# Kernel optimization log

Measured on AMD Instinct MI355X. Metric: run time of the kernel, lower is better.

Reference implementation:

```python
import jax, jax.numpy as jnp
import numpy as np

IMG = 256      # image size implied by 8x8 grid * scale 32
THRE = 0.5
DIS = 4        # img_dislocate_size
B = 64


def _shift_map(s, size, dis):
    # Pixel-level coordinate map for the dislocated half: cell r starts at
    # max(r*s - dis, 0) (the torch while-loop clamps negative coords to 0).
    p = jnp.arange(size)
    base = jnp.maximum((p // s) * s - dis, 0)
    return base + p % s


def _cell_norm(x, g, s):
    # Per-cell (crop) min/max normalization, matching the per-crop
    # (t - min) / (max - min + 1e-5) in HeatMaptoImg.
    b = x.shape[0]
    v = x.reshape(b, 1, g, s, g, s)
    mn = v.min(axis=(3, 5), keepdims=True)
    mx = v.max(axis=(3, 5), keepdims=True)
    return ((v - mn) / (mx - mn + 1e-5)).reshape(b, 1, g * s, g * s)


def setup_inputs() -> dict:
    key = jax.random.key(0)
    ks = jax.random.split(key, 7)
    B2 = 2 * B
    return {
        "img": jax.random.uniform(ks[0], (B, 1, IMG, IMG), jnp.float32),
        "heat8": jax.random.uniform(ks[1], (B2, 1, 8, 8), jnp.float32),
        "heat16": jax.random.uniform(ks[2], (B2, 1, 16, 16), jnp.float32),
        "heat32": jax.random.uniform(ks[3], (B2, 1, 32, 32), jnp.float32),
        "seg8": jax.random.uniform(ks[4], (B2, 1, IMG, IMG), jnp.float32),
        "seg16": jax.random.uniform(ks[5], (B2, 1, IMG, IMG), jnp.float32),
        "seg32": jax.random.uniform(ks[6], (B2, 1, IMG, IMG), jnp.float32),
    }


def reference(img, heat8, heat16, heat32, seg8, seg16, seg32):
    Bv = img.shape[0]
    label = jnp.zeros((Bv, 1, IMG, IMG), img.dtype)
    cnt = jnp.zeros_like(label)
    crops = {}
    # fine grid (scale 8) processed first, matching the reversed loop order
    for heat, seg, g in ((heat32, seg32, 32), (heat16, seg16, 16), (heat8, seg8, 8)):
        s = IMG // g                      # crop / cell size for this scale
        mask = (heat > THRE).astype(img.dtype)          # (2B,1,g,g)
        mask_pix = jnp.repeat(jnp.repeat(mask, s, axis=2), s, axis=3)  # (2B,1,256,256)
        Y = _shift_map(s, IMG, DIS)
        # dislocated half crops come from the shifted image region
        img_d = img[:, :, Y[:, None], Y[None, :]]       # (B,1,256,256)
        both = jnp.concatenate([img, img_d], axis=0)    # (2B,1,256,256)
        crops[g] = _cell_norm(both, g, s) * mask_pix
        # UnitLabels: scatter-add per-crop labels + counts, then average
        ca = mask_pix[:Bv]
        label = label + ca * seg[:Bv]
        cnt = cnt + ca
        cd = mask_pix[Bv:]
        label = label.at[:, :, Y[:, None], Y[None, :]].add(cd * seg[Bv:])
        cnt = cnt.at[:, :, Y[:, None], Y[None, :]].add(cd)
    label = label / (cnt + 1e-10)
    return (crops[32], crops[16], crops[8], label)
```

## Files before the change

### kernel.cpp

```cpp
#include <hip/hip_runtime.h>

#define IMG   256
#define IMG2  65536
#define NB    64
#define NB2   128

#define NBLK_C8   2048
#define NBLK_C16  1024
#define NBLK_C32  512
#define NBLK_LBL  4096
#define NBLK_ALL  (NBLK_C8 + NBLK_C16 + NBLK_C32 + NBLK_LBL)

template <int S>
__device__ __forceinline__ void crops_cell_row(
    const float* __restrict__ img,
    const float* __restrict__ heat,
    float* __restrict__ out,
    int src, int ci,
    float (*s_red)[32][4],
    float (*s_fin)[4]) {
    constexpr int G   = IMG / S;
    constexpr int L   = (S == 8) ? 3 : (S == 16) ? 4 : 5;
    constexpr int CPL = S / 4;

    const int tid = threadIdx.x;
    const int w   = tid >> 6;
    const int l   = tid & 63;
    const int cj  = l >> (L - 2);
    const int o   = (l & (CPL - 1)) * 4;

    const int rA   = ci * S;
    const int rB   = (ci == 0) ? 0 : rA - 4;
    const int colA = cj * S + o;
    const int colB = ((cj == 0) ? 0 : cj * S - 4) + o;

    const float* __restrict__ sp = img + (size_t)src * IMG2;

    float mnA = 3.4e38f, mxA = -3.4e38f, mnB = 3.4e38f, mxB = -3.4e38f;
#pragma unroll
    for (int k = 0; k < S / 4; ++k) {
        const int r = w + 4 * k;
        const float4 a  = *(const float4*)(sp + (rA + r) * IMG + colA);
        const float4 bq = *(const float4*)(sp + (rB + r) * IMG + colB);
        mnA = fminf(mnA, fminf(fminf(a.x, a.y), fminf(a.z, a.w)));
        mxA = fmaxf(mxA, fmaxf(fmaxf(a.x, a.y), fmaxf(a.z, a.w)));
        mnB = fminf(mnB, fminf(fminf(bq.x, bq.y), fminf(bq.z, bq.w)));
        mxB = fmaxf(mxB, fmaxf(fmaxf(bq.x, bq.y), fmaxf(bq.z, bq.w)));
    }
#pragma unroll
    for (int off = 1; off < CPL; off <<= 1) {
        mnA = fminf(mnA, __shfl_xor(mnA, off, 64));
        mxA = fmaxf(mxA, __shfl_xor(mxA, off, 64));
        mnB = fminf(mnB, __shfl_xor(mnB, off, 64));
        mxB = fmaxf(mxB, __shfl_xor(mxB, off, 64));
    }
    if ((l & (CPL - 1)) == 0) {
        float* p = &s_red[w][cj][0];
        p[0] = mnA; p[1] = mxA; p[2] = mnB; p[3] = mxB;
    }
    __syncthreads();
    if (tid < G) {
        float a0 = 3.4e38f, a1 = -3.4e38f, b0 = 3.4e38f, b1 = -3.4e38f;
#pragma unroll
        for (int ww = 0; ww < 4; ++ww) {
            a0 = fminf(a0, s_red[ww][tid][0]);
            a1 = fmaxf(a1, s_red[ww][tid][1]);
            b0 = fminf(b0, s_red[ww][tid][2]);
            b1 = fmaxf(b1, s_red[ww][tid][3]);
        }
        const float hA = heat[(size_t)src * G * G + ci * G + tid];
        const float hB = heat[(size_t)(src + NB) * G * G + ci * G + tid];
        s_fin[tid][0] = a0;
        s_fin[tid][1] = (hA > 0.5f ? 1.0f : 0.0f) / (a1 - a0 + 1e-5f);
        s_fin[tid][2] = b0;
        s_fin[tid][3] = (hB > 0.5f ? 1.0f : 0.0f) / (b1 - b0 + 1e-5f);
    }
    __syncthreads();
    const float fmnA = s_fin[cj][0], finvA = s_fin[cj][1];
    const float fmnB = s_fin[cj][2], finvB = s_fin[cj][3];

    float* __restrict__ dA = out + (size_t)src * IMG2;
    float* __restrict__ dB = out + (size_t)(src + NB) * IMG2;
#pragma unroll
    for (int k = 0; k < S / 4; ++k) {
        const int r = w + 4 * k;
        const float4 a  = *(const float4*)(sp + (rA + r) * IMG + colA);
        const float4 bq = *(const float4*)(sp + (rB + r) * IMG + colB);
        float4 oa, ob;
        oa.x = (a.x - fmnA) * finvA;  oa.y = (a.y - fmnA) * finvA;
        oa.z = (a.z - fmnA) * finvA;  oa.w = (a.w - fmnA) * finvA;
        ob.x = (bq.x - fmnB) * finvB; ob.y = (bq.y - fmnB) * finvB;
        ob.z = (bq.z - fmnB) * finvB; ob.w = (bq.w - fmnB) * finvB;
        *(float4*)(dA + (rA + r) * IMG + colA) = oa;
        *(float4*)(dB + (rA + r) * IMG + colA) = ob;
    }
}

__device__ __forceinline__ void label_rows(
    const float* __restrict__ heat8,
    const float* __restrict__ heat16,
    const float* __restrict__ heat32,
    const float* __restrict__ seg8,
    const float* __restrict__ seg16,
    const float* __restrict__ seg32,
    float* __restrict__ out,
    int b, int u0) {
    const int wave = threadIdx.x >> 6;
    const int lane = threadIdx.x & 63;
    const int u    = u0 + wave;
    const int v0   = lane << 2;
    const int vs   = min(v0 + 4, 252);

    float nu[4] = {0.f, 0.f, 0.f, 0.f};
    float de[4] = {0.f, 0.f, 0.f, 0.f};

    if (u0 >= 32 && u0 <= 248) {
        const int i1 = u + 4;
#define SCALE_F(heat, seg, g, l, s)                                           \
        {                                                                     \
            const float* __restrict__ h1 = heat + b * (g * g);                \
            const float* __restrict__ h2 = heat + (NB + b) * (g * g);         \
            const float* __restrict__ r1 = seg + (size_t)b * IMG2 + u * IMG;  \
            const float* __restrict__ r2 =                                    \
                seg + (size_t)(NB + b) * IMG2 + i1 * IMG;                     \
            const float4 sd  = *(const float4*)(r1 + v0);                     \
            const float4 sg0 = *(const float4*)(r2 + v0);                     \
            const float4 sg1 = *(const float4*)(r2 + vs);                     \
            const float hd  = h1[(u >> l) * g + (v0 >> l)];                   \
            const float hg0 = h2[(i1 >> l) * g + (v0 >> l)];                  \
            const float hg1 = h2[(i1 >> l) * g + (vs >> l)];                  \
            const float md = (hd > 0.5f) ? 1.0f : 0.0f;                       \
            const float g0 = (hg0 > 0.5f) ? 1.0f : 0.0f;                      \
            const float g1 = (hg1 > 0.5f) ? 1.0f : 0.0f;                      \
            _Pragma("unroll")                                                 \
            for (int c = 0; c < 4; ++c) {                                     \
                const int v = v0 + c;                                         \
                const float m0 = (v < (s)) ? g0 : 0.0f;                       \
                const float m1 = (v >= (s) - 4 && v <= 251) ? g1 : 0.0f;      \
                float x = ((const float*)&sd)[c] * md;                        \
                x = fmaf(m0, ((const float*)&sg0)[c], x);                     \
                x = fmaf(m1, ((const float*)&sg1)[c], x);                     \
                nu[c] += x;                                                   \
                de[c] += md + m0 + m1;                                        \
            }                                                                 \
        }
        SCALE_F(heat32, seg32, 32, 3, 8)
        SCALE_F(heat16, seg16, 16, 4, 16)
        SCALE_F(heat8,  seg8,  8,  5, 32)
#undef SCALE_F
    } else {
        const int i0  = u;
        const int i1c = min(u + 4, 255);
#define SCALE_G(heat, seg, g, l, s)                                           \
        {                                                                     \
            const float* __restrict__ h1 = heat + b * (g * g);                \
            const float* __restrict__ h2 = heat + (NB + b) * (g * g);         \
            const float* __restrict__ r1 = seg + (size_t)b * IMG2 + u * IMG;  \
            const float* __restrict__ ra =                                    \
                seg + (size_t)(NB + b) * IMG2 + i0 * IMG;                     \
            const float* __restrict__ rb =                                    \
                seg + (size_t)(NB + b) * IMG2 + i1c * IMG;                    \
            const float4 sd  = *(const float4*)(r1 + v0);                     \
            const float4 a0q = *(const float4*)(ra + v0);                     \
            const float4 a1q = *(const float4*)(ra + vs);                     \
            const float4 b0q = *(const float4*)(rb + v0);                     \
            const float4 b1q = *(const float4*)(rb + vs);                     \
            const float hd  = h1[(u >> l) * g + (v0 >> l)];                   \
            const float hA0 = h2[(i0 >> l) * g + (v0 >> l)];                  \
            const float hA1 = h2[(i0 >> l) * g + (vs >> l)];                  \
            const float hB0 = h2[(i1c >> l) * g + (v0 >> l)];                 \
            const float hB1 = h2[(i1c >> l) * g + (vs >> l)];                 \
            const float miA = (u < (s)) ? 1.0f : 0.0f;                        \
            const float miB = (u >= (s) - 4 && u <= 251) ? 1.0f : 0.0f;       \
            const float md  = (hd > 0.5f) ? 1.0f : 0.0f;                      \
            const float gA0 = miA * ((hA0 > 0.5f) ? 1.0f : 0.0f);             \
            const float gA1 = miA * ((hA1 > 0.5f) ? 1.0f : 0.0f);             \
            const float gB0 = miB * ((hB0 > 0.5f) ? 1.0f : 0.0f);             \
            const float gB1 = miB * ((hB1 > 0.5f) ? 1.0f : 0.0f);             \
            _Pragma("unroll")                                                 \
            for (int c = 0; c < 4; ++c) {                                     \
                const int v = v0 + c;                                         \
                const float mj0 = (v < (s)) ? 1.0f : 0.0f;                    \
                const float mj1 = (v >= (s) - 4 && v <= 251) ? 1.0f : 0.0f;   \
                const float w00 = gA0 * mj0, w01 = gA1 * mj1;                 \
                const float w10 = gB0 * mj0, w11 = gB1 * mj1;                 \
                float x = ((const float*)&sd)[c] * md;                        \
                x = fmaf(w00, ((const float*)&a0q)[c], x);                    \
                x = fmaf(w01, ((const float*)&a1q)[c], x);                    \
                x = fmaf(w10, ((const float*)&b0q)[c], x);                    \
                x = fmaf(w11, ((const float*)&b1q)[c], x);                    \
                nu[c] += x;                                                   \
                de[c] += md + w00 + w01 + w10 + w11;                          \
            }                                                                 \
        }
        SCALE_G(heat32, seg32, 32, 3, 8)
        SCALE_G(heat16, seg16, 16, 4, 16)
        SCALE_G(heat8,  seg8,  8,  5, 32)
#undef SCALE_G
    }

    float4 o;
    o.x = nu[0] / (de[0] + 1e-10f);
    o.y = nu[1] / (de[1] + 1e-10f);
    o.z = nu[2] / (de[2] + 1e-10f);
    o.w = nu[3] / (de[3] + 1e-10f);
    *(float4*)(out + (size_t)b * IMG2 + u * IMG + v0) = o;
}

__global__ __launch_bounds__(256) void fused_kernel(
    const float* __restrict__ img,
    const float* __restrict__ heat8,
    const float* __restrict__ heat16,
    const float* __restrict__ heat32,
    const float* __restrict__ seg8,
    const float* __restrict__ seg16,
    const float* __restrict__ seg32,
    float* __restrict__ out) {
    __shared__ float s_red[4][32][4];
    __shared__ float s_fin[32][4];

    float* crops32 = out;
    float* crops16 = out + (size_t)NB2 * IMG2;
    float* crops8  = out + (size_t)2 * NB2 * IMG2;
    float* label   = out + (size_t)3 * NB2 * IMG2;

    const int bid = blockIdx.x;
    if (bid < NBLK_C8) {
        crops_cell_row<8>(img, heat32, crops32, bid >> 5, bid & 31, s_red, s_fin);
    } else if (bid < NBLK_C8 + NBLK_C16) {
        const int t = bid - NBLK_C8;
        crops_cell_row<16>(img, heat16, crops16, t >> 4, t & 15, s_red, s_fin);
    } else if (bid < NBLK_C8 + NBLK_C16 + NBLK_C32) {
        const int t = bid - (NBLK_C8 + NBLK_C16);
        crops_cell_row<32>(img, heat8, crops8, t >> 3, t & 7, s_red, s_fin);
    } else {
        const int t = bid - (NBLK_C8 + NBLK_C16 + NBLK_C32);
        label_rows(heat8, heat16, heat32, seg8, seg16, seg32, label,
                   t >> 6, (t & 63) << 2);
    }
}

extern "C" void kernel_launch(void* const* d_in, const int* in_sizes, int n_in,
                              void* d_out, int out_size, void* d_ws, size_t ws_size,
                              hipStream_t stream) {
    const float* img    = (const float*)d_in[0];
    const float* heat8  = (const float*)d_in[1];
    const float* heat16 = (const float*)d_in[2];
    const float* heat32 = (const float*)d_in[3];
    const float* seg8   = (const float*)d_in[4];
    const float* seg16  = (const float*)d_in[5];
    const float* seg32  = (const float*)d_in[6];

    fused_kernel<<<dim3(NBLK_ALL), 256, 0, stream>>>(
        img, heat8, heat16, heat32, seg8, seg16, seg32, (float*)d_out);
}
```

Measured before the change: 224.5 us.

## Interleave crop and label blocks, use nontemporal stores, raise occupancy hint

Remaps block indices so each group of 15 blocks mixes 7 crop-normalization blocks with 8 label blocks. This balances the read-heavy label work and the store-heavy crop work across the machine at the same time instead of running them as separate phases. All output writes become nontemporal vector stores so the streamed outputs do not pollute cache. The launch bounds add a minimum of 8 blocks per CU, which may force register limits or spills.

New measurement: 234.1 us. +4.3%, slower.

```diff
diff --git a/kernel.cpp b/kernel.cpp
--- a/kernel.cpp
+++ b/kernel.cpp
@@ -4,6 +4,13 @@
 #define IMG2  65536
 #define NB    64
 #define NB2   128
+
+typedef float v4f __attribute__((ext_vector_type(4)));
+
+__device__ __forceinline__ void nt_store4(float* p, float x, float y, float z, float w) {
+    v4f v = {x, y, z, w};
+    __builtin_nontemporal_store(v, (v4f*)p);
+}
 
 #define NBLK_C8   2048
 #define NBLK_C16  1024
@@ -86,13 +93,12 @@
         const int r = w + 4 * k;
         const float4 a  = *(const float4*)(sp + (rA + r) * IMG + colA);
         const float4 bq = *(const float4*)(sp + (rB + r) * IMG + colB);
-        float4 oa, ob;
-        oa.x = (a.x - fmnA) * finvA;  oa.y = (a.y - fmnA) * finvA;
-        oa.z = (a.z - fmnA) * finvA;  oa.w = (a.w - fmnA) * finvA;
-        ob.x = (bq.x - fmnB) * finvB; ob.y = (bq.y - fmnB) * finvB;
-        ob.z = (bq.z - fmnB) * finvB; ob.w = (bq.w - fmnB) * finvB;
-        *(float4*)(dA + (rA + r) * IMG + colA) = oa;
-        *(float4*)(dB + (rA + r) * IMG + colA) = ob;
+        nt_store4(dA + (rA + r) * IMG + colA,
+                  (a.x - fmnA) * finvA, (a.y - fmnA) * finvA,
+                  (a.z - fmnA) * finvA, (a.w - fmnA) * finvA);
+        nt_store4(dB + (rA + r) * IMG + colA,
+                  (bq.x - fmnB) * finvB, (bq.y - fmnB) * finvB,
+                  (bq.z - fmnB) * finvB, (bq.w - fmnB) * finvB);
     }
 }
 
@@ -199,15 +205,12 @@
 #undef SCALE_G
     }
 
-    float4 o;
-    o.x = nu[0] / (de[0] + 1e-10f);
-    o.y = nu[1] / (de[1] + 1e-10f);
-    o.z = nu[2] / (de[2] + 1e-10f);
-    o.w = nu[3] / (de[3] + 1e-10f);
-    *(float4*)(out + (size_t)b * IMG2 + u * IMG + v0) = o;
-}
-
-__global__ __launch_bounds__(256) void fused_kernel(
+    nt_store4(out + (size_t)b * IMG2 + u * IMG + v0,
+              nu[0] / (de[0] + 1e-10f), nu[1] / (de[1] + 1e-10f),
+              nu[2] / (de[2] + 1e-10f), nu[3] / (de[3] + 1e-10f));
+}
+
+__global__ __launch_bounds__(256, 8) void fused_kernel(
     const float* __restrict__ img,
     const float* __restrict__ heat8,
     const float* __restrict__ heat16,
@@ -225,18 +228,24 @@
     float* label   = out + (size_t)3 * NB2 * IMG2;
 
     const int bid = blockIdx.x;
-    if (bid < NBLK_C8) {
-        crops_cell_row<8>(img, heat32, crops32, bid >> 5, bid & 31, s_red, s_fin);
-    } else if (bid < NBLK_C8 + NBLK_C16) {
-        const int t = bid - NBLK_C8;
-        crops_cell_row<16>(img, heat16, crops16, t >> 4, t & 15, s_red, s_fin);
-    } else if (bid < NBLK_C8 + NBLK_C16 + NBLK_C32) {
-        const int t = bid - (NBLK_C8 + NBLK_C16);
-        crops_cell_row<32>(img, heat8, crops8, t >> 3, t & 7, s_red, s_fin);
+    const int grp = bid / 15;
+    const int rem = bid - grp * 15;
+
+    if (rem < 7) {
+        const int cid = grp * 7 + rem;
+        if (cid < NBLK_C8) {
+            crops_cell_row<8>(img, heat32, crops32, cid >> 5, cid & 31, s_red, s_fin);
+        } else if (cid < NBLK_C8 + NBLK_C16) {
+            const int t = cid - NBLK_C8;
+            crops_cell_row<16>(img, heat16, crops16, t >> 4, t & 15, s_red, s_fin);
+        } else {
+            const int t = cid - (NBLK_C8 + NBLK_C16);
+            crops_cell_row<32>(img, heat8, crops8, t >> 3, t & 7, s_red, s_fin);
+        }
     } else {
-        const int t = bid - (NBLK_C8 + NBLK_C16 + NBLK_C32);
+        const int lid = grp * 8 + (rem - 7);
         label_rows(heat8, heat16, heat32, seg8, seg16, seg32, label,
-                   t >> 6, (t & 63) << 2);
+                   lid >> 6, (lid & 63) << 2);
     }
 }
 
```

## Map each crop cell to one wavefront and interleave crop and label blocks

Applied to the files above, without the earlier changes.

Rewrites the crop normalization so that each 64-lane wavefront owns a whole cell, or a group of cells for scale 8. Min/max is reduced with wave shuffles only, which removes shared memory and the block-level __syncthreads. Loaded values stay in registers for the normalize pass instead of being read from global memory twice. The block schedule is also interleaved, 9 crop blocks then 4 label blocks in every group of 13, to mix memory-heavy work across the GPU. This raises register pressure in the scale-32 path, and the block-index arithmetic has to cover exactly 13312 blocks.

Result: no change. 224.2 us (-0.1%).

```diff
diff --git a/kernel.cpp b/kernel.cpp
--- a/kernel.cpp
+++ b/kernel.cpp
@@ -5,94 +5,146 @@
 #define NB    64
 #define NB2   128
 
-#define NBLK_C8   2048
-#define NBLK_C16  1024
-#define NBLK_C32  512
-#define NBLK_LBL  4096
-#define NBLK_ALL  (NBLK_C8 + NBLK_C16 + NBLK_C32 + NBLK_LBL)
-
-template <int S>
-__device__ __forceinline__ void crops_cell_row(
-    const float* __restrict__ img,
-    const float* __restrict__ heat,
-    float* __restrict__ out,
-    int src, int ci,
-    float (*s_red)[32][4],
-    float (*s_fin)[4]) {
-    constexpr int G   = IMG / S;
-    constexpr int L   = (S == 8) ? 3 : (S == 16) ? 4 : 5;
-    constexpr int CPL = S / 4;
-
-    const int tid = threadIdx.x;
-    const int w   = tid >> 6;
-    const int l   = tid & 63;
-    const int cj  = l >> (L - 2);
-    const int o   = (l & (CPL - 1)) * 4;
-
-    const int rA   = ci * S;
-    const int rB   = (ci == 0) ? 0 : rA - 4;
-    const int colA = cj * S + o;
-    const int colB = ((cj == 0) ? 0 : cj * S - 4) + o;
+#define NBLK_ALL  13312
+
+__device__ __forceinline__ float4 norm4(float4 a, float mn, float inv) {
+    float4 o;
+    o.x = (a.x - mn) * inv; o.y = (a.y - mn) * inv;
+    o.z = (a.z - mn) * inv; o.w = (a.w - mn) * inv;
+    return o;
+}
+
+__device__ __forceinline__ void mm4(float4 a, float& mn, float& mx) {
+    mn = fminf(mn, fminf(fminf(a.x, a.y), fminf(a.z, a.w)));
+    mx = fmaxf(mx, fmaxf(fmaxf(a.x, a.y), fmaxf(a.z, a.w)));
+}
+
+__device__ __forceinline__ void crops_s8(
+    const float* __restrict__ img, const float* __restrict__ heat,
+    float* __restrict__ out, int wid) {
+    const int l   = threadIdx.x & 63;
+    const int src = wid >> 8;
+    const int rem = wid & 255;
+    const int ci  = rem >> 3;
+    const int st  = rem & 7;
+
+    const int r    = l >> 3;
+    const int cj   = st * 4 + ((l >> 1) & 3);
+    const int o    = (l & 1) * 4;
+    const int rowA = ci * 8 + r;
+    const int rowB = ((ci == 0) ? 0 : ci * 8 - 4) + r;
+    const int colA = st * 32 + (l & 7) * 4;
+    const int colB = ((cj == 0) ? 0 : cj * 8 - 4) + o;
 
     const float* __restrict__ sp = img + (size_t)src * IMG2;
+    const float4 a  = *(const float4*)(sp + rowA * IMG + colA);
+    const float4 bq = *(const float4*)(sp + rowB * IMG + colB);
 
     float mnA = 3.4e38f, mxA = -3.4e38f, mnB = 3.4e38f, mxB = -3.4e38f;
-#pragma unroll
-    for (int k = 0; k < S / 4; ++k) {
-        const int r = w + 4 * k;
-        const float4 a  = *(const float4*)(sp + (rA + r) * IMG + colA);
-        const float4 bq = *(const float4*)(sp + (rB + r) * IMG + colB);
-        mnA = fminf(mnA, fminf(fminf(a.x, a.y), fminf(a.z, a.w)));
-        mxA = fmaxf(mxA, fmaxf(fmaxf(a.x, a.y), fmaxf(a.z, a.w)));
-        mnB = fminf(mnB, fminf(fminf(bq.x, bq.y), fminf(bq.z, bq.w)));
-        mxB = fmaxf(mxB, fmaxf(fmaxf(bq.x, bq.y), fmaxf(bq.z, bq.w)));
-    }
-#pragma unroll
-    for (int off = 1; off < CPL; off <<= 1) {
+    mm4(a, mnA, mxA); mm4(bq, mnB, mxB);
+#pragma unroll
+    for (int k = 0; k < 4; ++k) {
+        const int off = (k == 0) ? 1 : (4 << k);
         mnA = fminf(mnA, __shfl_xor(mnA, off, 64));
         mxA = fmaxf(mxA, __shfl_xor(mxA, off, 64));
         mnB = fminf(mnB, __shfl_xor(mnB, off, 64));
         mxB = fmaxf(mxB, __shfl_xor(mxB, off, 64));
     }
-    if ((l & (CPL - 1)) == 0) {
-        float* p = &s_red[w][cj][0];
-        p[0] = mnA; p[1] = mxA; p[2] = mnB; p[3] = mxB;
-    }
-    __syncthreads();
-    if (tid < G) {
-        float a0 = 3.4e38f, a1 = -3.4e38f, b0 = 3.4e38f, b1 = -3.4e38f;
-#pragma unroll
-        for (int ww = 0; ww < 4; ++ww) {
-            a0 = fminf(a0, s_red[ww][tid][0]);
-            a1 = fmaxf(a1, s_red[ww][tid][1]);
-            b0 = fminf(b0, s_red[ww][tid][2]);
-            b1 = fmaxf(b1, s_red[ww][tid][3]);
-        }
-        const float hA = heat[(size_t)src * G * G + ci * G + tid];
-        const float hB = heat[(size_t)(src + NB) * G * G + ci * G + tid];
-        s_fin[tid][0] = a0;
-        s_fin[tid][1] = (hA > 0.5f ? 1.0f : 0.0f) / (a1 - a0 + 1e-5f);
-        s_fin[tid][2] = b0;
-        s_fin[tid][3] = (hB > 0.5f ? 1.0f : 0.0f) / (b1 - b0 + 1e-5f);
-    }
-    __syncthreads();
-    const float fmnA = s_fin[cj][0], finvA = s_fin[cj][1];
-    const float fmnB = s_fin[cj][2], finvB = s_fin[cj][3];
+    const float hA = heat[(size_t)src * 1024 + ci * 32 + cj];
+    const float hB = heat[(size_t)(src + NB) * 1024 + ci * 32 + cj];
+    const float invA = (hA > 0.5f ? 1.0f : 0.0f) / (mxA - mnA + 1e-5f);
+    const float invB = (hB > 0.5f ? 1.0f : 0.0f) / (mxB - mnB + 1e-5f);
+
+    const size_t p = (size_t)src * IMG2 + rowA * IMG + colA;
+    *(float4*)(out + p)                      = norm4(a,  mnA, invA);
+    *(float4*)(out + p + (size_t)NB * IMG2)  = norm4(bq, mnB, invB);
+}
+
+__device__ __forceinline__ void crops_s16(
+    const float* __restrict__ img, const float* __restrict__ heat,
+    float* __restrict__ out, int wid) {
+    const int l   = threadIdx.x & 63;
+    const int src = wid >> 8;
+    const int rem = wid & 255;
+    const int ci  = rem >> 4;
+    const int cj  = rem & 15;
+
+    const int r    = l >> 2;
+    const int o    = (l & 3) * 4;
+    const int rowA = ci * 16 + r;
+    const int rowB = ((ci == 0) ? 0 : ci * 16 - 4) + r;
+    const int colA = cj * 16 + o;
+    const int colB = ((cj == 0) ? 0 : cj * 16 - 4) + o;
+
+    const float* __restrict__ sp = img + (size_t)src * IMG2;
+    const float4 a  = *(const float4*)(sp + rowA * IMG + colA);
+    const float4 bq = *(const float4*)(sp + rowB * IMG + colB);
+
+    float mnA = 3.4e38f, mxA = -3.4e38f, mnB = 3.4e38f, mxB = -3.4e38f;
+    mm4(a, mnA, mxA); mm4(bq, mnB, mxB);
+#pragma unroll
+    for (int off = 1; off < 64; off <<= 1) {
+        mnA = fminf(mnA, __shfl_xor(mnA, off, 64));
+        mxA = fmaxf(mxA, __shfl_xor(mxA, off, 64));
+        mnB = fminf(mnB, __shfl_xor(mnB, off, 64));
+        mxB = fmaxf(mxB, __shfl_xor(mxB, off, 64));
+    }
+    const float hA = heat[(size_t)src * 256 + ci * 16 + cj];
+    const float hB = heat[(size_t)(src + NB) * 256 + ci * 16 + cj];
+    const float invA = (hA > 0.5f ? 1.0f : 0.0f) / (mxA - mnA + 1e-5f);
+    const float invB = (hB > 0.5f ? 1.0f : 0.0f) / (mxB - mnB + 1e-5f);
+
+    const size_t p = (size_t)src * IMG2 + rowA * IMG + colA;
+    *(float4*)(out + p)                      = norm4(a,  mnA, invA);
+    *(float4*)(out + p + (size_t)NB * IMG2)  = norm4(bq, mnB, invB);
+}
+
+__device__ __forceinline__ void crops_s32(
+    const float* __restrict__ img, const float* __restrict__ heat,
+    float* __restrict__ out, int wid) {
+    const int l   = threadIdx.x & 63;
+    const int src = wid >> 6;
+    const int rem = wid & 63;
+    const int ci  = rem >> 3;
+    const int cj  = rem & 7;
+
+    const int r0   = l >> 3;
+    const int o    = (l & 7) * 4;
+    const int rA   = ci * 32;
+    const int rB   = (ci == 0) ? 0 : rA - 4;
+    const int colA = cj * 32 + o;
+    const int colB = ((cj == 0) ? 0 : cj * 32 - 4) + o;
+
+    const float* __restrict__ sp = img + (size_t)src * IMG2;
+    float4 a[4], bq[4];
+#pragma unroll
+    for (int k = 0; k < 4; ++k) {
+        const int r = r0 + 8 * k;
+        a[k]  = *(const float4*)(sp + (rA + r) * IMG + colA);
+        bq[k] = *(const float4*)(sp + (rB + r) * IMG + colB);
+    }
+    float mnA = 3.4e38f, mxA = -3.4e38f, mnB = 3.4e38f, mxB = -3.4e38f;
+#pragma unroll
+    for (int k = 0; k < 4; ++k) { mm4(a[k], mnA, mxA); mm4(bq[k], mnB, mxB); }
+#pragma unroll
+    for (int off = 1; off < 64; off <<= 1) {
+        mnA = fminf(mnA, __shfl_xor(mnA, off, 64));
+        mxA = fmaxf(mxA, __shfl_xor(mxA, off, 64));
+        mnB = fminf(mnB, __shfl_xor(mnB, off, 64));
+        mxB = fmaxf(mxB, __shfl_xor(mxB, off, 64));
+    }
+    const float hA = heat[(size_t)src * 64 + ci * 8 + cj];
+    const float hB = heat[(size_t)(src + NB) * 64 + ci * 8 + cj];
+    const float invA = (hA > 0.5f ? 1.0f : 0.0f) / (mxA - mnA + 1e-5f);
+    const float invB = (hB > 0.5f ? 1.0f : 0.0f) / (mxB - mnB + 1e-5f);
 
     float* __restrict__ dA = out + (size_t)src * IMG2;
     float* __restrict__ dB = out + (size_t)(src + NB) * IMG2;
 #pragma unroll
-    for (int k = 0; k < S / 4; ++k) {
-        const int r = w + 4 * k;
-        const float4 a  = *(const float4*)(sp + (rA + r) * IMG + colA);
-        const float4 bq = *(const float4*)(sp + (rB + r) * IMG + colB);
-        float4 oa, ob;
-        oa.x = (a.x - fmnA) * finvA;  oa.y = (a.y - fmnA) * finvA;
-        oa.z = (a.z - fmnA) * finvA;  oa.w = (a.w - fmnA) * finvA;
-        ob.x = (bq.x - fmnB) * finvB; ob.y = (bq.y - fmnB) * finvB;
-        ob.z = (bq.z - fmnB) * finvB; ob.w = (bq.w - fmnB) * finvB;
-        *(float4*)(dA + (rA + r) * IMG + colA) = oa;
-        *(float4*)(dB + (rA + r) * IMG + colA) = ob;
+    for (int k = 0; k < 4; ++k) {
+        const int r = r0 + 8 * k;
+        *(float4*)(dA + (rA + r) * IMG + colA) = norm4(a[k],  mnA, invA);
+        *(float4*)(dB + (rA + r) * IMG + colA) = norm4(bq[k], mnB, invB);
     }
 }
 
@@ -216,27 +268,29 @@
     const float* __restrict__ seg16,
     const float* __restrict__ seg32,
     float* __restrict__ out) {
-    __shared__ float s_red[4][32][4];
-    __shared__ float s_fin[32][4];
-
     float* crops32 = out;
     float* crops16 = out + (size_t)NB2 * IMG2;
     float* crops8  = out + (size_t)2 * NB2 * IMG2;
     float* label   = out + (size_t)3 * NB2 * IMG2;
 
     const int bid = blockIdx.x;
-    if (bid < NBLK_C8) {
-        crops_cell_row<8>(img, heat32, crops32, bid >> 5, bid & 31, s_red, s_fin);
-    } else if (bid < NBLK_C8 + NBLK_C16) {
-        const int t = bid - NBLK_C8;
-        crops_cell_row<16>(img, heat16, crops16, t >> 4, t & 15, s_red, s_fin);
-    } else if (bid < NBLK_C8 + NBLK_C16 + NBLK_C32) {
-        const int t = bid - (NBLK_C8 + NBLK_C16);
-        crops_cell_row<32>(img, heat8, crops8, t >> 3, t & 7, s_red, s_fin);
+    const int grp = bid / 13;
+    const int rem = bid - grp * 13;
+
+    if (rem < 9) {
+        const int cb  = grp * 9 + rem;
+        const int wid = cb * 4 + (threadIdx.x >> 6);
+        if (cb < 4096) {
+            crops_s8(img, heat32, crops32, wid);
+        } else if (cb < 8192) {
+            crops_s16(img, heat16, crops16, wid - 16384);
+        } else {
+            crops_s32(img, heat8, crops8, wid - 32768);
+        }
     } else {
-        const int t = bid - (NBLK_C8 + NBLK_C16 + NBLK_C32);
+        const int lid = grp * 4 + (rem - 9);
         label_rows(heat8, heat16, heat32, seg8, seg16, seg32, label,
-                   t >> 6, (t & 63) << 2);
+                   lid >> 6, (lid & 63) << 2);
     }
 }
 
```

## Split crops into stats pass plus row-streaming normalize kernel, separate label kernel

Applied to the files above, without the earlier changes.

Replaces the per-cell-row crops blocks with two stages. A stats kernel computes per-cell min and scaled inverse range into workspace, one thread per cell. A row-streaming kernel then reads each image row once and writes the normalized outputs for all three scales. The label work moves into its own launch. This trades one fused launch for three launches plus a workspace round trip, aiming for fully coalesced row-wise writes and fewer redundant image reads. The stats kernel's one-thread-per-cell serial loops (up to 32x32 values per thread) could be slow and poorly coalesced.

Result: slower. 250.3 us (+11.5%).

```diff
diff --git a/kernel.cpp b/kernel.cpp
--- a/kernel.cpp
+++ b/kernel.cpp
@@ -5,95 +5,119 @@
 #define NB    64
 #define NB2   128
 
-#define NBLK_C8   2048
-#define NBLK_C16  1024
-#define NBLK_C32  512
-#define NBLK_LBL  4096
-#define NBLK_ALL  (NBLK_C8 + NBLK_C16 + NBLK_C32 + NBLK_LBL)
-
-template <int S>
-__device__ __forceinline__ void crops_cell_row(
+
+#define WS_A8   0
+#define WS_B8   65536
+#define WS_A16  131072
+#define WS_B16  147456
+#define WS_A32  163840
+#define WS_B32  167936
+
+template <int S, int G>
+__device__ __forceinline__ void cell_stats(
+    const float* __restrict__ img, const float* __restrict__ heat,
+    float2* __restrict__ ws, int idx, int half, int wsbase) {
+    const int b  = idx / (G * G);
+    const int rr = idx % (G * G);
+    const int ci = rr / G;
+    const int cj = rr % G;
+    const int r0 = half ? max(ci * S - 4, 0) : ci * S;
+    const int c0 = half ? max(cj * S - 4, 0) : cj * S;
+    const float* __restrict__ p = img + (size_t)b * IMG2 + r0 * IMG + c0;
+    float mn = 3.4e38f, mx = -3.4e38f;
+    for (int r = 0; r < S; ++r) {
+#pragma unroll
+        for (int c = 0; c < S; c += 4) {
+            const float4 q = *(const float4*)(p + r * IMG + c);
+            mn = fminf(mn, fminf(fminf(q.x, q.y), fminf(q.z, q.w)));
+            mx = fmaxf(mx, fmaxf(fmaxf(q.x, q.y), fmaxf(q.z, q.w)));
+        }
+    }
+    const float h   = heat[(size_t)(b + half * NB) * (G * G) + ci * G + cj];
+    const float inv = (h > 0.5f ? 1.0f : 0.0f) / (mx - mn + 1e-5f);
+    ws[wsbase + idx] = make_float2(mn, inv);
+}
+
+__global__ __launch_bounds__(256) void stats_kernel(
     const float* __restrict__ img,
-    const float* __restrict__ heat,
-    float* __restrict__ out,
-    int src, int ci,
-    float (*s_red)[32][4],
-    float (*s_fin)[4]) {
-    constexpr int G   = IMG / S;
-    constexpr int L   = (S == 8) ? 3 : (S == 16) ? 4 : 5;
-    constexpr int CPL = S / 4;
-
-    const int tid = threadIdx.x;
-    const int w   = tid >> 6;
-    const int l   = tid & 63;
-    const int cj  = l >> (L - 2);
-    const int o   = (l & (CPL - 1)) * 4;
-
-    const int rA   = ci * S;
-    const int rB   = (ci == 0) ? 0 : rA - 4;
-    const int colA = cj * S + o;
-    const int colB = ((cj == 0) ? 0 : cj * S - 4) + o;
-
-    const float* __restrict__ sp = img + (size_t)src * IMG2;
-
-    float mnA = 3.4e38f, mxA = -3.4e38f, mnB = 3.4e38f, mxB = -3.4e38f;
-#pragma unroll
-    for (int k = 0; k < S / 4; ++k) {
-        const int r = w + 4 * k;
-        const float4 a  = *(const float4*)(sp + (rA + r) * IMG + colA);
-        const float4 bq = *(const float4*)(sp + (rB + r) * IMG + colB);
-        mnA = fminf(mnA, fminf(fminf(a.x, a.y), fminf(a.z, a.w)));
-        mxA = fmaxf(mxA, fmaxf(fmaxf(a.x, a.y), fmaxf(a.z, a.w)));
-        mnB = fminf(mnB, fminf(fminf(bq.x, bq.y), fminf(bq.z, bq.w)));
-        mxB = fmaxf(mxB, fmaxf(fmaxf(bq.x, bq.y), fmaxf(bq.z, bq.w)));
+    const float* __restrict__ heat8,
+    const float* __restrict__ heat16,
+    const float* __restrict__ heat32,
+    float2* __restrict__ ws) {
+    const int t = blockIdx.x * 256 + threadIdx.x;
+    if (t < 131072) {
+        const int half = t >> 16;
+        cell_stats<8, 32>(img, heat32, ws, t & 65535, half,
+                          half ? WS_B8 : WS_A8);
+    } else if (t < 163840) {
+        const int tt = t - 131072;
+        const int half = tt >> 14;
+        cell_stats<16, 16>(img, heat16, ws, tt & 16383, half,
+                           half ? WS_B16 : WS_A16);
+    } else {
+        const int tt = t - 163840;
+        const int half = tt >> 12;
+        cell_stats<32, 8>(img, heat8, ws, tt & 4095, half,
+                          half ? WS_B32 : WS_A32);
     }
-#pragma unroll
-    for (int off = 1; off < CPL; off <<= 1) {
-        mnA = fminf(mnA, __shfl_xor(mnA, off, 64));
-        mxA = fmaxf(mxA, __shfl_xor(mxA, off, 64));
-        mnB = fminf(mnB, __shfl_xor(mnB, off, 64));
-        mxB = fmaxf(mxB, __shfl_xor(mxB, off, 64));
-    }
-    if ((l & (CPL - 1)) == 0) {
-        float* p = &s_red[w][cj][0];
-        p[0] = mnA; p[1] = mxA; p[2] = mnB; p[3] = mxB;
-    }
-    __syncthreads();
-    if (tid < G) {
-        float a0 = 3.4e38f, a1 = -3.4e38f, b0 = 3.4e38f, b1 = -3.4e38f;
-#pragma unroll
-        for (int ww = 0; ww < 4; ++ww) {
-            a0 = fminf(a0, s_red[ww][tid][0]);
-            a1 = fmaxf(a1, s_red[ww][tid][1]);
-            b0 = fminf(b0, s_red[ww][tid][2]);
-            b1 = fmaxf(b1, s_red[ww][tid][3]);
-        }
-        const float hA = heat[(size_t)src * G * G + ci * G + tid];
-        const float hB = heat[(size_t)(src + NB) * G * G + ci * G + tid];
-        s_fin[tid][0] = a0;
-        s_fin[tid][1] = (hA > 0.5f ? 1.0f : 0.0f) / (a1 - a0 + 1e-5f);
-        s_fin[tid][2] = b0;
-        s_fin[tid][3] = (hB > 0.5f ? 1.0f : 0.0f) / (b1 - b0 + 1e-5f);
-    }
-    __syncthreads();
-    const float fmnA = s_fin[cj][0], finvA = s_fin[cj][1];
-    const float fmnB = s_fin[cj][2], finvB = s_fin[cj][3];
-
-    float* __restrict__ dA = out + (size_t)src * IMG2;
-    float* __restrict__ dB = out + (size_t)(src + NB) * IMG2;
-#pragma unroll
-    for (int k = 0; k < S / 4; ++k) {
-        const int r = w + 4 * k;
-        const float4 a  = *(const float4*)(sp + (rA + r) * IMG + colA);
-        const float4 bq = *(const float4*)(sp + (rB + r) * IMG + colB);
-        float4 oa, ob;
-        oa.x = (a.x - fmnA) * finvA;  oa.y = (a.y - fmnA) * finvA;
-        oa.z = (a.z - fmnA) * finvA;  oa.w = (a.w - fmnA) * finvA;
-        ob.x = (bq.x - fmnB) * finvB; ob.y = (bq.y - fmnB) * finvB;
-        ob.z = (bq.z - fmnB) * finvB; ob.w = (bq.w - fmnB) * finvB;
-        *(float4*)(dA + (rA + r) * IMG + colA) = oa;
-        *(float4*)(dB + (rA + r) * IMG + colA) = ob;
-    }
+}
+
+__device__ __forceinline__ float4 nrm(float4 q, float2 st) {
+    float4 o;
+    o.x = (q.x - st.x) * st.y; o.y = (q.y - st.x) * st.y;
+    o.z = (q.z - st.x) * st.y; o.w = (q.w - st.x) * st.y;
+    return o;
+}
+
+__global__ __launch_bounds__(256) void crops_stream_kernel(
+    const float* __restrict__ img,
+    const float2* __restrict__ ws,
+    float* __restrict__ out) {
+    const int w    = threadIdx.x >> 6;
+    const int lane = threadIdx.x & 63;
+    const int lid  = blockIdx.x * 4 + w;
+    const int b    = lid >> 8;
+    const int u    = lid & 255;
+    const int v0   = lane << 2;
+    const int vm   = max(v0 - 4, 0);
+
+    const float* __restrict__ ip = img + (size_t)b * IMG2;
+
+    const int u8  = ((u >> 3) ? (u & ~7)  - 4 : 0) + (u & 7);
+    const int u16 = ((u >> 4) ? (u & ~15) - 4 : 0) + (u & 15);
+    const int u32 = ((u >> 5) ? (u & ~31) - 4 : 0) + (u & 31);
+
+    const float4 xa  = *(const float4*)(ip + u   * IMG + v0);
+    const float4 q08 = *(const float4*)(ip + u8  * IMG + v0);
+    const float4 qm8 = *(const float4*)(ip + u8  * IMG + vm);
+    const float4 q16 = *(const float4*)(ip + u16 * IMG + v0);
+    const float4 qm6 = *(const float4*)(ip + u16 * IMG + vm);
+    const float4 q32 = *(const float4*)(ip + u32 * IMG + v0);
+    const float4 qm2 = *(const float4*)(ip + u32 * IMG + vm);
+
+    const float2 a8  = ws[WS_A8  + ((b << 5) + (u >> 3)) * 32 + (v0 >> 3)];
+    const float2 b8  = ws[WS_B8  + ((b << 5) + (u >> 3)) * 32 + (v0 >> 3)];
+    const float2 a16 = ws[WS_A16 + ((b << 4) + (u >> 4)) * 16 + (v0 >> 4)];
+    const float2 b16 = ws[WS_B16 + ((b << 4) + (u >> 4)) * 16 + (v0 >> 4)];
+    const float2 a32 = ws[WS_A32 + ((b << 3) + (u >> 5)) *  8 + (v0 >> 5)];
+    const float2 b32 = ws[WS_B32 + ((b << 3) + (u >> 5)) *  8 + (v0 >> 5)];
+
+    const float4 s8v = (v0 < 8)  ? q08 : qm8;
+    const float4 s16v = (v0 < 16) ? q16 : qm6;
+    const float4 s32v = (v0 < 32) ? q32 : qm2;
+
+    const size_t rowA = (size_t)b * IMG2 + u * IMG + v0;
+    const size_t rowB = (size_t)(b + NB) * IMG2 + u * IMG + v0;
+    float* __restrict__ c32 = out;
+    float* __restrict__ c16 = out + (size_t)NB2 * IMG2;
+    float* __restrict__ c8  = out + (size_t)2 * NB2 * IMG2;
+
+    *(float4*)(c32 + rowA) = nrm(xa,  a8);
+    *(float4*)(c32 + rowB) = nrm(s8v, b8);
+    *(float4*)(c16 + rowA) = nrm(xa,  a16);
+    *(float4*)(c16 + rowB) = nrm(s16v, b16);
+    *(float4*)(c8  + rowA) = nrm(xa,  a32);
+    *(float4*)(c8  + rowB) = nrm(s32v, b32);
 }
 
 __device__ __forceinline__ void label_rows(
@@ -207,8 +231,7 @@
     *(float4*)(out + (size_t)b * IMG2 + u * IMG + v0) = o;
 }
 
-__global__ __launch_bounds__(256) void fused_kernel(
-    const float* __restrict__ img,
+__global__ __launch_bounds__(256) void label_kernel(
     const float* __restrict__ heat8,
     const float* __restrict__ heat16,
     const float* __restrict__ heat32,
@@ -216,28 +239,10 @@
     const float* __restrict__ seg16,
     const float* __restrict__ seg32,
     float* __restrict__ out) {
-    __shared__ float s_red[4][32][4];
-    __shared__ float s_fin[32][4];
-
-    float* crops32 = out;
-    float* crops16 = out + (size_t)NB2 * IMG2;
-    float* crops8  = out + (size_t)2 * NB2 * IMG2;
-    float* label   = out + (size_t)3 * NB2 * IMG2;
-
-    const int bid = blockIdx.x;
-    if (bid < NBLK_C8) {
-        crops_cell_row<8>(img, heat32, crops32, bid >> 5, bid & 31, s_red, s_fin);
-    } else if (bid < NBLK_C8 + NBLK_C16) {
-        const int t = bid - NBLK_C8;
-        crops_cell_row<16>(img, heat16, crops16, t >> 4, t & 15, s_red, s_fin);
-    } else if (bid < NBLK_C8 + NBLK_C16 + NBLK_C32) {
-        const int t = bid - (NBLK_C8 + NBLK_C16);
-        crops_cell_row<32>(img, heat8, crops8, t >> 3, t & 7, s_red, s_fin);
-    } else {
-        const int t = bid - (NBLK_C8 + NBLK_C16 + NBLK_C32);
-        label_rows(heat8, heat16, heat32, seg8, seg16, seg32, label,
-                   t >> 6, (t & 63) << 2);
-    }
+    float* label = out + (size_t)3 * NB2 * IMG2;
+    const int t  = blockIdx.x;
+    label_rows(heat8, heat16, heat32, seg8, seg16, seg32, label,
+               t >> 6, (t & 63) << 2);
 }
 
 extern "C" void kernel_launch(void* const* d_in, const int* in_sizes, int n_in,
@@ -251,6 +256,10 @@
     const float* seg16  = (const float*)d_in[5];
     const float* seg32  = (const float*)d_in[6];
 
-    fused_kernel<<<dim3(NBLK_ALL), 256, 0, stream>>>(
-        img, heat8, heat16, heat32, seg8, seg16, seg32, (float*)d_out);
-}
+    stats_kernel<<<dim3(672), 256, 0, stream>>>(
+        img, heat8, heat16, heat32, (float2*)d_ws);
+    crops_stream_kernel<<<dim3(4096), 256, 0, stream>>>(
+        img, (const float2*)d_ws, (float*)d_out);
+    label_kernel<<<dim3(4096), 256, 0, stream>>>(
+        heat8, heat16, heat32, seg8, seg16, seg32, (float*)d_out);
+}
```
